# Kernel tuning notes

Measured on AMD Instinct MI355X. Metric: run time of the kernel, lower is better.

Reference implementation:

```python
import jax, jax.numpy as jnp
import numpy as np
import math

R1 = 1.0
R2 = 4.0
NBINS_XY = 4
NBINS_ZY = 4
PARTITIONS = NBINS_XY * NBINS_ZY * 2  # 32
TOPK = 200
TWO_PI = 2.0 * math.pi
PI = math.pi


def setup_inputs() -> dict:
    key = jax.random.key(0)
    k1, k2 = jax.random.split(key)
    # LiDAR-like coordinates, ~[-30, 30] meters
    sampled_vehicle_points = jax.random.normal(k1, (1024, 3), dtype=jnp.float32) * 20.0
    fusion_point = jax.random.normal(k2, (20000, 3), dtype=jnp.float32) * 20.0
    return {"sampled_vehicle_points": sampled_vehicle_points, "fusion_point": fusion_point}


def _compute_partitions_batch(q):
    # q: [S, K, 3]. rel[b, i, j] = q[b, j] - q[b, i]  (A.unsqueeze(1) - B.unsqueeze(2))
    rel = q[:, None, :, :] - q[:, :, None, :]  # [S, K, K, 3]
    angles_xy = jnp.fmod(jnp.arctan2(rel[..., 1], rel[..., 0]) + TWO_PI, TWO_PI)
    angles_zy = jnp.fmod(jnp.arctan2(rel[..., 1], rel[..., 2]) + TWO_PI, PI)
    xy_bins = jnp.floor(angles_xy / (TWO_PI / NBINS_XY))
    zy_bins = jnp.floor(angles_zy / (PI / NBINS_ZY))
    # hash(A, B, seed=NBINS_ZY): -1 where either < 0
    angle_ok = (xy_bins >= 0) & (zy_bins >= 0)
    angles_bins = jnp.where(angle_ok, xy_bins * NBINS_ZY + zy_bins, -1.0)
    D = jnp.sqrt(jnp.sum(rel * rel, axis=-1) + 1e-7)  # [S, K, K]
    dist_bins = jnp.where(D >= R2, 1.0, jnp.where(D >= R1, 0.0, -1.0))
    bin_ok = (dist_bins >= 0) & (angles_bins >= 0)
    bins = jnp.where(bin_ok, dist_bins * (NBINS_XY * NBINS_ZY) + angles_bins, -1.0)
    return bins  # [S, K, K] float, -1 for ignored


def reference(sampled_vehicle_points, fusion_point):
    # kNN query: K nearest fusion points for each sampled vehicle point
    d2 = jnp.sum(
        (sampled_vehicle_points[:, None, :] - fusion_point[None, :, :]) ** 2, axis=-1
    )  # [S, Nf]
    _, idx = jax.lax.top_k(-d2, TOPK)  # indices of TOPK smallest distances
    queried = fusion_point[idx]  # [S, K, 3]

    bins = _compute_partitions_batch(queried)  # [S, K, K]
    row0 = bins[:, 0, :]  # [S, K] — only row 0 is used by the loss
    # points_in_partition[s, p] = sum_j (row0[s, j] == p) + 1
    counts = jnp.sum(
        row0[:, :, None] == jnp.arange(PARTITIONS, dtype=bins.dtype)[None, None, :],
        axis=1,
    ).astype(jnp.float32) + 1.0  # [S, P]
    pip = counts / jnp.linalg.norm(counts, axis=-1, keepdims=True) * 4.0
    gt_dist = jax.nn.softmax(pip, axis=-1)
    return gt_dist
```

## Files before the change

kernel.cpp:

```cpp
#include <hip/hip_runtime.h>
#include <math.h>

#define KTOP 200
#define NPART 32
#define BLOCK 512
#define NHIST 2048
#define CAND_CAP 512
#define WCAP 512
#define MAXIT 10

__device__ __forceinline__ float d2_ref(float ax, float ay, float az,
                                        float bx, float by, float bz) {
    float dx = __fsub_rn(ax, bx), dy = __fsub_rn(ay, by), dz = __fsub_rn(az, bz);
    return __fadd_rn(__fadd_rn(__fmul_rn(dx, dx), __fmul_rn(dy, dy)), __fmul_rn(dz, dz));
}

__device__ __forceinline__ unsigned key_of(const float* __restrict__ fus, int j,
                                           float vx, float vy, float vz) {
    return __float_as_uint(d2_ref(vx, vy, vz, fus[3*j], fus[3*j+1], fus[3*j+2]));
}

__device__ __forceinline__ int compute_bin(float rx, float ry, float rz) {
    const float TWO_PI_F = (float)6.283185307179586;
    const float PI_F     = (float)3.141592653589793;
    const float XY_W     = (float)(6.283185307179586 / 4.0);
    const float ZY_W     = (float)(3.141592653589793 / 4.0);

    float d2 = __fadd_rn(__fadd_rn(__fmul_rn(rx, rx), __fmul_rn(ry, ry)), __fmul_rn(rz, rz));
    float D  = sqrtf(__fadd_rn(d2, 1e-7f));
    float dist_bin;
    if (D >= 4.0f)      dist_bin = 1.0f;
    else if (D >= 1.0f) dist_bin = 0.0f;
    else                return -1;

    float axy = fmodf(atan2f(ry, rx) + TWO_PI_F, TWO_PI_F);
    float azy = fmodf(atan2f(ry, rz) + TWO_PI_F, PI_F);
    float xyb = floorf(__fdiv_rn(axy, XY_W));
    float zyb = floorf(__fdiv_rn(azy, ZY_W));
    if (!(xyb >= 0.0f && zyb >= 0.0f)) return -1;
    float ab  = xyb * 4.0f + zyb;
    int bin = (int)(dist_bin * 16.0f + ab);
    return bin;
}

__global__ __launch_bounds__(BLOCK, 8)
void shape_context_kernel(const float* __restrict__ veh,
                          const float* __restrict__ fus,
                          float* __restrict__ out,
                          int nfus) {
    const int b   = blockIdx.x;
    const int tid = threadIdx.x;
    const int lane = tid & 63;
    const int wid  = tid >> 6;

    __shared__ unsigned int hist[NHIST];
    __shared__ unsigned long long cand[CAND_CAP];
    __shared__ int wlist[WCAP];
    __shared__ unsigned int hist32[NPART];
    __shared__ unsigned int waveTot[BLOCK / 64];
    __shared__ unsigned int waveBase[BLOCK / 64];
    __shared__ unsigned int s_bucket, s_rem, s_bcount;
    __shared__ int s_candCount, s_wcount;
    __shared__ float s_q0[3];
    __shared__ unsigned long long s_minPacked, s_lowBound;

    const float vx = veh[b * 3 + 0], vy = veh[b * 3 + 1], vz = veh[b * 3 + 2];
    const float4* fus4 = (const float4*)fus;
    const int ntrip = nfus >> 2;

    if (tid == 0) { s_minPacked = ~0ull; s_candCount = 0; s_wcount = 0; }
    for (int i = tid; i < NHIST; i += BLOCK) hist[i] = 0;
    if (tid < NPART) hist32[tid] = 0;
    __syncthreads();

    auto find_bucket = [&](unsigned remq) {
        const int PER = NHIST / BLOCK;
        int base = tid * PER;
        unsigned p = 0;
        #pragma unroll
        for (int i = 0; i < PER; i++) p += hist[base + i];
        unsigned incl = p;
        #pragma unroll
        for (int d = 1; d < 64; d <<= 1) {
            unsigned n = __shfl_up(incl, d, 64);
            if (lane >= d) incl += n;
        }
        if (lane == 63) waveTot[wid] = incl;
        __syncthreads();
        if (tid == 0) {
            unsigned acc = 0;
            for (int w = 0; w < BLOCK / 64; w++) { waveBase[w] = acc; acc += waveTot[w]; }
        }
        __syncthreads();
        unsigned excl = waveBase[wid] + incl - p;
        if (excl < remq && remq <= excl + p) {
            unsigned cum = excl;
            #pragma unroll
            for (int i = 0; i < PER; i++) {
                unsigned c = hist[base + i];
                if (cum + c >= remq) { s_bucket = base + i; s_rem = remq - cum; s_bcount = c; break; }
                cum += c;
            }
        }
        __syncthreads();
    };

    unsigned long long khi[MAXIT];
    unsigned long long lmin = ~0ull;
    #pragma unroll
    for (int it = 0; it < MAXIT; ++it) {
        int m = tid + it * BLOCK;
        if (m < ntrip) {
            float4 A = fus4[3 * m], Bq = fus4[3 * m + 1], Cq = fus4[3 * m + 2];
            unsigned k0 = __float_as_uint(d2_ref(vx, vy, vz, A.x,  A.y,  A.z));
            unsigned k1 = __float_as_uint(d2_ref(vx, vy, vz, A.w,  Bq.x, Bq.y));
            unsigned k2 = __float_as_uint(d2_ref(vx, vy, vz, Bq.z, Bq.w, Cq.x));
            unsigned k3 = __float_as_uint(d2_ref(vx, vy, vz, Cq.y, Cq.z, Cq.w));
            atomicAdd(&hist[k0 >> 21], 1u);
            atomicAdd(&hist[k1 >> 21], 1u);
            atomicAdd(&hist[k2 >> 21], 1u);
            atomicAdd(&hist[k3 >> 21], 1u);
            khi[it] = (unsigned long long)(k0 >> 21)
                    | ((unsigned long long)(k1 >> 21) << 16)
                    | ((unsigned long long)(k2 >> 21) << 32)
                    | ((unsigned long long)(k3 >> 21) << 48);
            unsigned jb = 4 * m;
            unsigned long long p0 = ((unsigned long long)k0 << 32) | (jb + 0);
            unsigned long long p1 = ((unsigned long long)k1 << 32) | (jb + 1);
            unsigned long long p2 = ((unsigned long long)k2 << 32) | (jb + 2);
            unsigned long long p3 = ((unsigned long long)k3 << 32) | (jb + 3);
            unsigned long long pm = min(min(p0, p1), min(p2, p3));
            lmin = min(lmin, pm);
        } else {
            khi[it] = 0xFFFFFFFFFFFFFFFFull;
        }
    }
    for (int m = MAXIT * BLOCK + tid; m < ntrip; m += BLOCK) {
        #pragma unroll
        for (int q = 0; q < 4; ++q) {
            unsigned k = key_of(fus, 4 * m + q, vx, vy, vz);
            atomicAdd(&hist[k >> 21], 1u);
            lmin = min(lmin, ((unsigned long long)k << 32) | (unsigned)(4 * m + q));
        }
    }
    for (int j = (nfus & ~3) + tid; j < nfus; j += BLOCK) {
        unsigned k = key_of(fus, j, vx, vy, vz);
        atomicAdd(&hist[k >> 21], 1u);
        lmin = min(lmin, ((unsigned long long)k << 32) | (unsigned)j);
    }
    #pragma unroll
    for (int d = 32; d > 0; d >>= 1) {
        unsigned long long o = __shfl_xor(lmin, d, 64);
        lmin = (o < lmin) ? o : lmin;
    }
    if (lane == 0) atomicMin(&s_minPacked, lmin);
    __syncthreads();

    find_bucket(KTOP);
    unsigned T = s_bucket;
    unsigned rem = s_rem;
    unsigned bcount = s_bcount;
    int shift = 21;

    if (tid == 0) {
        int idx0 = (int)(s_minPacked & 0xFFFFFFFFull);
        s_q0[0] = fus[idx0 * 3]; s_q0[1] = fus[idx0 * 3 + 1]; s_q0[2] = fus[idx0 * 3 + 2];
    }
    __syncthreads();
    const float q0x = s_q0[0], q0y = s_q0[1], q0z = s_q0[2];

    while (bcount > CAND_CAP && shift > 0) {
        int newshift = (shift > 11) ? (shift - 11) : 0;
        unsigned digmask = (1u << (shift - newshift)) - 1;
        for (int i = tid; i < NHIST; i += BLOCK) hist[i] = 0;
        __syncthreads();
        for (int j = tid; j < nfus; j += BLOCK) {
            unsigned k = key_of(fus, j, vx, vy, vz);
            if ((k >> shift) == T) atomicAdd(&hist[(k >> newshift) & digmask], 1u);
        }
        __syncthreads();
        find_bucket(rem);
        T = (T << (shift - newshift)) | s_bucket;
        rem = s_rem;
        bcount = s_bcount;
        shift = newshift;
    }

    if (shift == 21) {
        #pragma unroll
        for (int it = 0; it < MAXIT; ++it) {
            unsigned long long packed = khi[it];
            int jb = 4 * (tid + it * BLOCK);
            #pragma unroll
            for (int q = 0; q < 4; ++q) {
                unsigned hi = (unsigned)((packed >> (16 * q)) & 0xFFFFull);
                if (hi < T) {
                    int pos = atomicAdd(&s_wcount, 1);
                    if (pos < WCAP) wlist[pos] = jb + q;
                } else if (hi == T) {
                    int j = jb + q;
                    unsigned k = key_of(fus, j, vx, vy, vz);
                    int pos = atomicAdd(&s_candCount, 1);
                    if (pos < CAND_CAP) cand[pos] = ((unsigned long long)k << 32) | (unsigned)j;
                }
            }
        }
        for (int m = MAXIT * BLOCK + tid; m < ntrip; m += BLOCK)
            #pragma unroll
            for (int q = 0; q < 4; ++q) {
                int j = 4 * m + q;
                unsigned k = key_of(fus, j, vx, vy, vz);
                unsigned hi = k >> shift;
                if (hi < T) { int pos = atomicAdd(&s_wcount, 1); if (pos < WCAP) wlist[pos] = j; }
                else if (hi == T) { int pos = atomicAdd(&s_candCount, 1); if (pos < CAND_CAP) cand[pos] = ((unsigned long long)k << 32) | (unsigned)j; }
            }
        for (int j = (nfus & ~3) + tid; j < nfus; j += BLOCK) {
            unsigned k = key_of(fus, j, vx, vy, vz);
            unsigned hi = k >> shift;
            if (hi < T) { int pos = atomicAdd(&s_wcount, 1); if (pos < WCAP) wlist[pos] = j; }
            else if (hi == T) { int pos = atomicAdd(&s_candCount, 1); if (pos < CAND_CAP) cand[pos] = ((unsigned long long)k << 32) | (unsigned)j; }
        }
    } else {
        for (int j = tid; j < nfus; j += BLOCK) {
            unsigned k = key_of(fus, j, vx, vy, vz);
            unsigned hi = k >> shift;
            if (hi < T) { int pos = atomicAdd(&s_wcount, 1); if (pos < WCAP) wlist[pos] = j; }
            else if (hi == T) { int pos = atomicAdd(&s_candCount, 1); if (pos < CAND_CAP) cand[pos] = ((unsigned long long)k << 32) | (unsigned)j; }
        }
    }
    __syncthreads();

    const int cnt = s_candCount;
    if (cnt <= CAND_CAP) {
        for (int i = tid; i < cnt; i += BLOCK) {
            unsigned long long me = cand[i];
            int rank = 0;
            for (int k2 = 0; k2 < cnt; k2++) rank += (cand[k2] < me) ? 1 : 0;
            if (rank < (int)rem) {
                int pos = atomicAdd(&s_wcount, 1);
                if (pos < WCAP) wlist[pos] = (int)(me & 0xFFFFFFFFull);
            }
        }
    }
    __syncthreads();

    {
        int wc = s_wcount; if (wc > WCAP) wc = WCAP;
        for (int i = tid; i < wc; i += BLOCK) {
            int j = wlist[i];
            float fx = fus[3 * j], fy = fus[3 * j + 1], fz = fus[3 * j + 2];
            int bin = compute_bin(__fsub_rn(fx, q0x), __fsub_rn(fy, q0y), __fsub_rn(fz, q0z));
            if (bin >= 0 && bin < NPART) atomicAdd(&hist32[bin], 1u);
        }
    }
    __syncthreads();

    if (cnt > CAND_CAP) {
        if (tid == 0) s_lowBound = 0;
        __syncthreads();
        for (unsigned itx = 0; itx < rem; ++itx) {
            if (tid == 0) s_minPacked = ~0ull;
            __syncthreads();
            unsigned long long lowB = s_lowBound;
            unsigned long long lm = ~0ull;
            for (int j = tid; j < nfus; j += BLOCK) {
                unsigned k = key_of(fus, j, vx, vy, vz);
                if ((k >> shift) == T) {
                    unsigned long long p = ((unsigned long long)k << 32) | (unsigned)j;
                    if (p >= lowB && p < lm) lm = p;
                }
            }
            #pragma unroll
            for (int d = 32; d > 0; d >>= 1) {
                unsigned long long o = __shfl_xor(lm, d, 64);
                lm = (o < lm) ? o : lm;
            }
            if (lane == 0) atomicMin(&s_minPacked, lm);
            __syncthreads();
            if (tid == 0) {
                int jm = (int)(s_minPacked & 0xFFFFFFFFull);
                float fx = fus[jm * 3], fy = fus[jm * 3 + 1], fz = fus[jm * 3 + 2];
                int bin = compute_bin(__fsub_rn(fx, q0x), __fsub_rn(fy, q0y), __fsub_rn(fz, q0z));
                if (bin >= 0 && bin < NPART) hist32[bin] += 1u;
                s_lowBound = s_minPacked + 1;
            }
            __syncthreads();
        }
    }

    if (tid < NPART) {
        float c = (float)hist32[tid] + 1.0f;
        float ss = __fmul_rn(c, c);
        #pragma unroll
        for (int d = 16; d > 0; d >>= 1) ss += __shfl_xor(ss, d, 64);
        float v = __fmul_rn(__fdiv_rn(c, sqrtf(ss)), 4.0f);
        float mx = v;
        #pragma unroll
        for (int d = 16; d > 0; d >>= 1) mx = fmaxf(mx, __shfl_xor(mx, d, 64));
        float e = expf(v - mx);
        float sum = e;
        #pragma unroll
        for (int d = 16; d > 0; d >>= 1) sum += __shfl_xor(sum, d, 64);
        out[b * NPART + tid] = __fdiv_rn(e, sum);
    }
}

extern "C" void kernel_launch(void* const* d_in, const int* in_sizes, int n_in,
                              void* d_out, int out_size, void* d_ws, size_t ws_size,
                              hipStream_t stream) {
    const float* veh = (const float*)d_in[0];
    const float* fus = (const float*)d_in[1];
    float* out = (float*)d_out;
    int nveh = in_sizes[0] / 3;
    int nfus = in_sizes[1] / 3;
    shape_context_kernel<<<nveh, BLOCK, 0, stream>>>(veh, fus, out, nfus);
}
```

Measured before the change: 82.68 us.

## Split histogram per half-wave and derive nearest point from first bucket

Duplicates the shared-memory radix histogram into two copies selected by the upper half of each wave, which spreads out atomic contention. The per-element 64-bit running minimum in the main pass is dropped. The nearest point is instead found after the histogram pass by rescanning only elements in the first non-empty bucket with shared atomicMin. The candidate cap is also raised to 1024 so the refinement passes trigger less often, at the cost of more shared memory and a larger rank sort.

```diff
diff --git a/kernel.cpp b/kernel.cpp
--- a/kernel.cpp
+++ b/kernel.cpp
@@ -5,7 +5,8 @@
 #define NPART 32
 #define BLOCK 512
 #define NHIST 2048
-#define CAND_CAP 512
+#define HOFF 2049
+#define CAND_CAP 1024
 #define WCAP 512
 #define MAXIT 10
 
@@ -53,32 +54,33 @@
     const int lane = tid & 63;
     const int wid  = tid >> 6;
 
-    __shared__ unsigned int hist[NHIST];
+    __shared__ unsigned int hist[2 * NHIST + 1];
     __shared__ unsigned long long cand[CAND_CAP];
     __shared__ int wlist[WCAP];
     __shared__ unsigned int hist32[NPART];
     __shared__ unsigned int waveTot[BLOCK / 64];
     __shared__ unsigned int waveBase[BLOCK / 64];
-    __shared__ unsigned int s_bucket, s_rem, s_bcount;
+    __shared__ unsigned int s_bucket, s_rem, s_bcount, s_b0;
     __shared__ int s_candCount, s_wcount;
-    __shared__ float s_q0[3];
     __shared__ unsigned long long s_minPacked, s_lowBound;
 
     const float vx = veh[b * 3 + 0], vy = veh[b * 3 + 1], vz = veh[b * 3 + 2];
     const float4* fus4 = (const float4*)fus;
     const int ntrip = nfus >> 2;
+    const int hoff = (lane & 32) ? HOFF : 0;
 
     if (tid == 0) { s_minPacked = ~0ull; s_candCount = 0; s_wcount = 0; }
-    for (int i = tid; i < NHIST; i += BLOCK) hist[i] = 0;
+    for (int i = tid; i < 2 * NHIST + 1; i += BLOCK) hist[i] = 0;
     if (tid < NPART) hist32[tid] = 0;
     __syncthreads();
 
     auto find_bucket = [&](unsigned remq) {
         const int PER = NHIST / BLOCK;
         int base = tid * PER;
+        unsigned c[PER];
         unsigned p = 0;
         #pragma unroll
-        for (int i = 0; i < PER; i++) p += hist[base + i];
+        for (int i = 0; i < PER; i++) { c[i] = hist[base + i] + hist[HOFF + base + i]; p += c[i]; }
         unsigned incl = p;
         #pragma unroll
         for (int d = 1; d < 64; d <<= 1) {
@@ -93,20 +95,22 @@
         }
         __syncthreads();
         unsigned excl = waveBase[wid] + incl - p;
+        if (excl == 0 && p > 0) {
+            #pragma unroll
+            for (int i = 0; i < PER; i++) if (c[i] > 0) { s_b0 = base + i; break; }
+        }
         if (excl < remq && remq <= excl + p) {
             unsigned cum = excl;
             #pragma unroll
             for (int i = 0; i < PER; i++) {
-                unsigned c = hist[base + i];
-                if (cum + c >= remq) { s_bucket = base + i; s_rem = remq - cum; s_bcount = c; break; }
-                cum += c;
+                if (cum + c[i] >= remq) { s_bucket = base + i; s_rem = remq - cum; s_bcount = c[i]; break; }
+                cum += c[i];
             }
         }
         __syncthreads();
     };
 
     unsigned long long khi[MAXIT];
-    unsigned long long lmin = ~0ull;
     #pragma unroll
     for (int it = 0; it < MAXIT; ++it) {
         int m = tid + it * BLOCK;
@@ -116,67 +120,67 @@
             unsigned k1 = __float_as_uint(d2_ref(vx, vy, vz, A.w,  Bq.x, Bq.y));
             unsigned k2 = __float_as_uint(d2_ref(vx, vy, vz, Bq.z, Bq.w, Cq.x));
             unsigned k3 = __float_as_uint(d2_ref(vx, vy, vz, Cq.y, Cq.z, Cq.w));
-            atomicAdd(&hist[k0 >> 21], 1u);
-            atomicAdd(&hist[k1 >> 21], 1u);
-            atomicAdd(&hist[k2 >> 21], 1u);
-            atomicAdd(&hist[k3 >> 21], 1u);
+            atomicAdd(&hist[hoff + (k0 >> 21)], 1u);
+            atomicAdd(&hist[hoff + (k1 >> 21)], 1u);
+            atomicAdd(&hist[hoff + (k2 >> 21)], 1u);
+            atomicAdd(&hist[hoff + (k3 >> 21)], 1u);
             khi[it] = (unsigned long long)(k0 >> 21)
                     | ((unsigned long long)(k1 >> 21) << 16)
                     | ((unsigned long long)(k2 >> 21) << 32)
                     | ((unsigned long long)(k3 >> 21) << 48);
-            unsigned jb = 4 * m;
-            unsigned long long p0 = ((unsigned long long)k0 << 32) | (jb + 0);
-            unsigned long long p1 = ((unsigned long long)k1 << 32) | (jb + 1);
-            unsigned long long p2 = ((unsigned long long)k2 << 32) | (jb + 2);
-            unsigned long long p3 = ((unsigned long long)k3 << 32) | (jb + 3);
-            unsigned long long pm = min(min(p0, p1), min(p2, p3));
-            lmin = min(lmin, pm);
         } else {
             khi[it] = 0xFFFFFFFFFFFFFFFFull;
         }
     }
-    for (int m = MAXIT * BLOCK + tid; m < ntrip; m += BLOCK) {
-        #pragma unroll
-        for (int q = 0; q < 4; ++q) {
-            unsigned k = key_of(fus, 4 * m + q, vx, vy, vz);
-            atomicAdd(&hist[k >> 21], 1u);
-            lmin = min(lmin, ((unsigned long long)k << 32) | (unsigned)(4 * m + q));
-        }
-    }
-    for (int j = (nfus & ~3) + tid; j < nfus; j += BLOCK) {
-        unsigned k = key_of(fus, j, vx, vy, vz);
-        atomicAdd(&hist[k >> 21], 1u);
-        lmin = min(lmin, ((unsigned long long)k << 32) | (unsigned)j);
-    }
-    #pragma unroll
-    for (int d = 32; d > 0; d >>= 1) {
-        unsigned long long o = __shfl_xor(lmin, d, 64);
-        lmin = (o < lmin) ? o : lmin;
-    }
-    if (lane == 0) atomicMin(&s_minPacked, lmin);
+    for (int m = MAXIT * BLOCK + tid; m < ntrip; m += BLOCK)
+        #pragma unroll
+        for (int q = 0; q < 4; ++q)
+            atomicAdd(&hist[hoff + (key_of(fus, 4 * m + q, vx, vy, vz) >> 21)], 1u);
+    for (int j = (nfus & ~3) + tid; j < nfus; j += BLOCK)
+        atomicAdd(&hist[hoff + (key_of(fus, j, vx, vy, vz) >> 21)], 1u);
     __syncthreads();
 
     find_bucket(KTOP);
     unsigned T = s_bucket;
     unsigned rem = s_rem;
     unsigned bcount = s_bcount;
+    const unsigned b0 = s_b0;
     int shift = 21;
 
-    if (tid == 0) {
-        int idx0 = (int)(s_minPacked & 0xFFFFFFFFull);
-        s_q0[0] = fus[idx0 * 3]; s_q0[1] = fus[idx0 * 3 + 1]; s_q0[2] = fus[idx0 * 3 + 2];
-    }
-    __syncthreads();
-    const float q0x = s_q0[0], q0y = s_q0[1], q0z = s_q0[2];
+    #pragma unroll
+    for (int it = 0; it < MAXIT; ++it) {
+        unsigned long long packed = khi[it];
+        int jb = 4 * (tid + it * BLOCK);
+        #pragma unroll
+        for (int q = 0; q < 4; ++q) {
+            unsigned hi = (unsigned)((packed >> (16 * q)) & 0xFFFFull);
+            if (hi == b0) {
+                int j = jb + q;
+                unsigned k = key_of(fus, j, vx, vy, vz);
+                atomicMin(&s_minPacked, ((unsigned long long)k << 32) | (unsigned)j);
+            }
+        }
+    }
+    for (int m = MAXIT * BLOCK + tid; m < ntrip; m += BLOCK)
+        #pragma unroll
+        for (int q = 0; q < 4; ++q) {
+            unsigned k = key_of(fus, 4 * m + q, vx, vy, vz);
+            if ((k >> 21) == b0) atomicMin(&s_minPacked, ((unsigned long long)k << 32) | (unsigned)(4 * m + q));
+        }
+    for (int j = (nfus & ~3) + tid; j < nfus; j += BLOCK) {
+        unsigned k = key_of(fus, j, vx, vy, vz);
+        if ((k >> 21) == b0) atomicMin(&s_minPacked, ((unsigned long long)k << 32) | (unsigned)j);
+    }
 
     while (bcount > CAND_CAP && shift > 0) {
         int newshift = (shift > 11) ? (shift - 11) : 0;
         unsigned digmask = (1u << (shift - newshift)) - 1;
-        for (int i = tid; i < NHIST; i += BLOCK) hist[i] = 0;
+        __syncthreads();
+        for (int i = tid; i < 2 * NHIST + 1; i += BLOCK) hist[i] = 0;
         __syncthreads();
         for (int j = tid; j < nfus; j += BLOCK) {
             unsigned k = key_of(fus, j, vx, vy, vz);
-            if ((k >> shift) == T) atomicAdd(&hist[(k >> newshift) & digmask], 1u);
+            if ((k >> shift) == T) atomicAdd(&hist[hoff + ((k >> newshift) & digmask)], 1u);
         }
         __syncthreads();
         find_bucket(rem);
@@ -244,6 +248,9 @@
     }
     __syncthreads();
 
+    const int idx0 = (int)(s_minPacked & 0xFFFFFFFFull);
+    const float q0x = fus[idx0 * 3], q0y = fus[idx0 * 3 + 1], q0z = fus[idx0 * 3 + 2];
+
     {
         int wc = s_wcount; if (wc > WCAP) wc = WCAP;
         for (int i = tid; i < wc; i += BLOCK) {
@@ -253,7 +260,6 @@
             if (bin >= 0 && bin < NPART) atomicAdd(&hist32[bin], 1u);
         }
     }
-    __syncthreads();
 
     if (cnt > CAND_CAP) {
         if (tid == 0) s_lowBound = 0;
@@ -287,6 +293,7 @@
             __syncthreads();
         }
     }
+    __syncthreads();
 
     if (tid < NPART) {
         float c = (float)hist32[tid] + 1.0f;
```

Result: slower. 88.51 us (+7.1%).

## Sample-based threshold prefilter for top-k selection replacing full histogram pass

Applied to the files above, without the earlier changes.

Builds a coarse histogram from 512 evenly spaced sample points and picks a threshold bucket expected to hold a little more than the 200 nearest points. One pass over all fusion points then keeps only candidates under that threshold, and selection (min, histogram on finer bits, rank) runs on that small set in shared memory. This removes the full-data histogram with its global atomics and the per-thread packed key registers. A fallback path repeats the old full radix-select if the candidate count falls outside [KTOP, CAND_CAP], at extra cost for unlucky inputs.

```diff
diff --git a/kernel.cpp b/kernel.cpp
--- a/kernel.cpp
+++ b/kernel.cpp
@@ -5,9 +5,10 @@
 #define NPART 32
 #define BLOCK 512
 #define NHIST 2048
-#define CAND_CAP 512
-#define WCAP 512
-#define MAXIT 10
+#define CAND_CAP 2048
+#define TLIST_CAP 1024
+#define WCAP 256
+#define SSTAR 28
 
 __device__ __forceinline__ float d2_ref(float ax, float ay, float az,
                                         float bx, float by, float bz) {
@@ -55,20 +56,20 @@
 
     __shared__ unsigned int hist[NHIST];
     __shared__ unsigned long long cand[CAND_CAP];
+    __shared__ unsigned long long tlist[TLIST_CAP];
     __shared__ int wlist[WCAP];
     __shared__ unsigned int hist32[NPART];
     __shared__ unsigned int waveTot[BLOCK / 64];
     __shared__ unsigned int waveBase[BLOCK / 64];
     __shared__ unsigned int s_bucket, s_rem, s_bcount;
-    __shared__ int s_candCount, s_wcount;
-    __shared__ float s_q0[3];
-    __shared__ unsigned long long s_minPacked, s_lowBound;
+    __shared__ int s_candCount, s_wcount, s_tcount;
+    __shared__ unsigned long long s_minPacked, s_serMin, s_lowBound;
 
     const float vx = veh[b * 3 + 0], vy = veh[b * 3 + 1], vz = veh[b * 3 + 2];
     const float4* fus4 = (const float4*)fus;
     const int ntrip = nfus >> 2;
 
-    if (tid == 0) { s_minPacked = ~0ull; s_candCount = 0; s_wcount = 0; }
+    if (tid == 0) { s_minPacked = ~0ull; s_candCount = 0; s_wcount = 0; s_tcount = 0; }
     for (int i = tid; i < NHIST; i += BLOCK) hist[i] = 0;
     if (tid < NPART) hist32[tid] = 0;
     __syncthreads();
@@ -76,9 +77,10 @@
     auto find_bucket = [&](unsigned remq) {
         const int PER = NHIST / BLOCK;
         int base = tid * PER;
+        unsigned c[PER];
         unsigned p = 0;
         #pragma unroll
-        for (int i = 0; i < PER; i++) p += hist[base + i];
+        for (int i = 0; i < PER; i++) { c[i] = hist[base + i]; p += c[i]; }
         unsigned incl = p;
         #pragma unroll
         for (int d = 1; d < 64; d <<= 1) {
@@ -97,153 +99,205 @@
             unsigned cum = excl;
             #pragma unroll
             for (int i = 0; i < PER; i++) {
-                unsigned c = hist[base + i];
-                if (cum + c >= remq) { s_bucket = base + i; s_rem = remq - cum; s_bcount = c; break; }
-                cum += c;
+                if (cum + c[i] >= remq) { s_bucket = base + i; s_rem = remq - cum; s_bcount = c[i]; break; }
+                cum += c[i];
             }
         }
         __syncthreads();
     };
 
-    unsigned long long khi[MAXIT];
-    unsigned long long lmin = ~0ull;
-    #pragma unroll
-    for (int it = 0; it < MAXIT; ++it) {
-        int m = tid + it * BLOCK;
-        if (m < ntrip) {
-            float4 A = fus4[3 * m], Bq = fus4[3 * m + 1], Cq = fus4[3 * m + 2];
-            unsigned k0 = __float_as_uint(d2_ref(vx, vy, vz, A.x,  A.y,  A.z));
-            unsigned k1 = __float_as_uint(d2_ref(vx, vy, vz, A.w,  Bq.x, Bq.y));
-            unsigned k2 = __float_as_uint(d2_ref(vx, vy, vz, Bq.z, Bq.w, Cq.x));
-            unsigned k3 = __float_as_uint(d2_ref(vx, vy, vz, Cq.y, Cq.z, Cq.w));
-            atomicAdd(&hist[k0 >> 21], 1u);
-            atomicAdd(&hist[k1 >> 21], 1u);
-            atomicAdd(&hist[k2 >> 21], 1u);
-            atomicAdd(&hist[k3 >> 21], 1u);
-            khi[it] = (unsigned long long)(k0 >> 21)
-                    | ((unsigned long long)(k1 >> 21) << 16)
-                    | ((unsigned long long)(k2 >> 21) << 32)
-                    | ((unsigned long long)(k3 >> 21) << 48);
-            unsigned jb = 4 * m;
-            unsigned long long p0 = ((unsigned long long)k0 << 32) | (jb + 0);
-            unsigned long long p1 = ((unsigned long long)k1 << 32) | (jb + 1);
-            unsigned long long p2 = ((unsigned long long)k2 << 32) | (jb + 2);
-            unsigned long long p3 = ((unsigned long long)k3 << 32) | (jb + 3);
-            unsigned long long pm = min(min(p0, p1), min(p2, p3));
-            lmin = min(lmin, pm);
-        } else {
-            khi[it] = 0xFFFFFFFFFFFFFFFFull;
-        }
-    }
-    for (int m = MAXIT * BLOCK + tid; m < ntrip; m += BLOCK) {
-        #pragma unroll
-        for (int q = 0; q < 4; ++q) {
-            unsigned k = key_of(fus, 4 * m + q, vx, vy, vz);
-            atomicAdd(&hist[k >> 21], 1u);
-            lmin = min(lmin, ((unsigned long long)k << 32) | (unsigned)(4 * m + q));
-        }
+    {
+        int j = (int)(((long long)tid * nfus) / BLOCK);
+        unsigned k = key_of(fus, j, vx, vy, vz);
+        atomicAdd(&hist[k >> 21], 1u);
+    }
+    __syncthreads();
+    find_bucket(SSTAR);
+    const unsigned Pb = s_bucket + 1;
+    __syncthreads();
+
+    for (int m = tid; m < ntrip; m += BLOCK) {
+        float4 A = fus4[3 * m], Bq = fus4[3 * m + 1], Cq = fus4[3 * m + 2];
+        unsigned k0 = __float_as_uint(d2_ref(vx, vy, vz, A.x,  A.y,  A.z));
+        unsigned k1 = __float_as_uint(d2_ref(vx, vy, vz, A.w,  Bq.x, Bq.y));
+        unsigned k2 = __float_as_uint(d2_ref(vx, vy, vz, Bq.z, Bq.w, Cq.x));
+        unsigned k3 = __float_as_uint(d2_ref(vx, vy, vz, Cq.y, Cq.z, Cq.w));
+        int jb = 4 * m;
+        if ((k0 >> 21) < Pb) { int pos = atomicAdd(&s_candCount, 1); if (pos < CAND_CAP) cand[pos] = ((unsigned long long)k0 << 32) | (unsigned)(jb + 0); }
+        if ((k1 >> 21) < Pb) { int pos = atomicAdd(&s_candCount, 1); if (pos < CAND_CAP) cand[pos] = ((unsigned long long)k1 << 32) | (unsigned)(jb + 1); }
+        if ((k2 >> 21) < Pb) { int pos = atomicAdd(&s_candCount, 1); if (pos < CAND_CAP) cand[pos] = ((unsigned long long)k2 << 32) | (unsigned)(jb + 2); }
+        if ((k3 >> 21) < Pb) { int pos = atomicAdd(&s_candCount, 1); if (pos < CAND_CAP) cand[pos] = ((unsigned long long)k3 << 32) | (unsigned)(jb + 3); }
     }
     for (int j = (nfus & ~3) + tid; j < nfus; j += BLOCK) {
         unsigned k = key_of(fus, j, vx, vy, vz);
-        atomicAdd(&hist[k >> 21], 1u);
-        lmin = min(lmin, ((unsigned long long)k << 32) | (unsigned)j);
-    }
-    #pragma unroll
-    for (int d = 32; d > 0; d >>= 1) {
-        unsigned long long o = __shfl_xor(lmin, d, 64);
-        lmin = (o < lmin) ? o : lmin;
-    }
-    if (lane == 0) atomicMin(&s_minPacked, lmin);
-    __syncthreads();
-
-    find_bucket(KTOP);
-    unsigned T = s_bucket;
-    unsigned rem = s_rem;
-    unsigned bcount = s_bcount;
-    int shift = 21;
-
-    if (tid == 0) {
-        int idx0 = (int)(s_minPacked & 0xFFFFFFFFull);
-        s_q0[0] = fus[idx0 * 3]; s_q0[1] = fus[idx0 * 3 + 1]; s_q0[2] = fus[idx0 * 3 + 2];
-    }
-    __syncthreads();
-    const float q0x = s_q0[0], q0y = s_q0[1], q0z = s_q0[2];
-
-    while (bcount > CAND_CAP && shift > 0) {
-        int newshift = (shift > 11) ? (shift - 11) : 0;
-        unsigned digmask = (1u << (shift - newshift)) - 1;
+        if ((k >> 21) < Pb) { int pos = atomicAdd(&s_candCount, 1); if (pos < CAND_CAP) cand[pos] = ((unsigned long long)k << 32) | (unsigned)j; }
+    }
+    __syncthreads();
+
+    const int cnt = s_candCount;
+    unsigned rem;
+
+    if (cnt >= KTOP && cnt <= CAND_CAP) {
+        unsigned long long lm = ~0ull;
+        for (int i = tid; i < cnt; i += BLOCK) lm = min(lm, cand[i]);
+        #pragma unroll
+        for (int d = 32; d > 0; d >>= 1) {
+            unsigned long long o = __shfl_xor(lm, d, 64);
+            lm = (o < lm) ? o : lm;
+        }
+        if (lane == 0) atomicMin(&s_minPacked, lm);
+
         for (int i = tid; i < NHIST; i += BLOCK) hist[i] = 0;
         __syncthreads();
-        for (int j = tid; j < nfus; j += BLOCK) {
-            unsigned k = key_of(fus, j, vx, vy, vz);
-            if ((k >> shift) == T) atomicAdd(&hist[(k >> newshift) & digmask], 1u);
-        }
-        __syncthreads();
-        find_bucket(rem);
-        T = (T << (shift - newshift)) | s_bucket;
+        for (int i = tid; i < cnt; i += BLOCK) atomicAdd(&hist[(unsigned)(cand[i] >> 53)], 1u);
+        __syncthreads();
+        find_bucket(KTOP);
+        const unsigned T2 = s_bucket;
         rem = s_rem;
-        bcount = s_bcount;
-        shift = newshift;
-    }
-
-    if (shift == 21) {
-        #pragma unroll
-        for (int it = 0; it < MAXIT; ++it) {
-            unsigned long long packed = khi[it];
-            int jb = 4 * (tid + it * BLOCK);
-            #pragma unroll
-            for (int q = 0; q < 4; ++q) {
-                unsigned hi = (unsigned)((packed >> (16 * q)) & 0xFFFFull);
-                if (hi < T) {
+        const unsigned bcount = s_bcount;
+
+        if (bcount <= TLIST_CAP) {
+            for (int i = tid; i < cnt; i += BLOCK) {
+                unsigned bk = (unsigned)(cand[i] >> 53);
+                if (bk < T2) {
                     int pos = atomicAdd(&s_wcount, 1);
-                    if (pos < WCAP) wlist[pos] = jb + q;
-                } else if (hi == T) {
-                    int j = jb + q;
-                    unsigned k = key_of(fus, j, vx, vy, vz);
-                    int pos = atomicAdd(&s_candCount, 1);
-                    if (pos < CAND_CAP) cand[pos] = ((unsigned long long)k << 32) | (unsigned)j;
-                }
-            }
-        }
-        for (int m = MAXIT * BLOCK + tid; m < ntrip; m += BLOCK)
-            #pragma unroll
-            for (int q = 0; q < 4; ++q) {
-                int j = 4 * m + q;
+                    if (pos < WCAP) wlist[pos] = (int)(cand[i] & 0xFFFFFFFFull);
+                } else if (bk == T2) {
+                    int pos = atomicAdd(&s_tcount, 1);
+                    if (pos < TLIST_CAP) tlist[pos] = cand[i];
+                }
+            }
+            __syncthreads();
+            const int tc = s_tcount;
+            for (int i = tid; i < tc; i += BLOCK) {
+                unsigned long long me = tlist[i];
+                int rank = 0;
+                for (int k2 = 0; k2 < tc; k2++) rank += (tlist[k2] < me) ? 1 : 0;
+                if (rank < (int)rem) {
+                    int pos = atomicAdd(&s_wcount, 1);
+                    if (pos < WCAP) wlist[pos] = (int)(me & 0xFFFFFFFFull);
+                }
+            }
+        } else {
+            for (int i = tid; i < cnt; i += BLOCK) {
+                unsigned bk = (unsigned)(cand[i] >> 53);
+                if (bk < T2) {
+                    int pos = atomicAdd(&s_wcount, 1);
+                    if (pos < WCAP) wlist[pos] = (int)(cand[i] & 0xFFFFFFFFull);
+                }
+            }
+            __syncthreads();
+            for (int i = tid; i < cnt; i += BLOCK) {
+                unsigned long long me = cand[i];
+                if ((unsigned)(me >> 53) == T2) {
+                    int rank = 0;
+                    for (int k2 = 0; k2 < cnt; k2++) {
+                        unsigned long long o = cand[k2];
+                        rank += ((unsigned)(o >> 53) == T2 && o < me) ? 1 : 0;
+                    }
+                    if (rank < (int)rem) {
+                        int pos = atomicAdd(&s_wcount, 1);
+                        if (pos < WCAP) wlist[pos] = (int)(me & 0xFFFFFFFFull);
+                    }
+                }
+            }
+        }
+        __syncthreads();
+    } else {
+        if (tid == 0) s_candCount = 0;
+        for (int i = tid; i < NHIST; i += BLOCK) hist[i] = 0;
+        __syncthreads();
+        for (int j = tid; j < nfus; j += BLOCK)
+            atomicAdd(&hist[key_of(fus, j, vx, vy, vz) >> 21], 1u);
+        __syncthreads();
+        find_bucket(KTOP);
+        unsigned T = s_bucket;
+        rem = s_rem;
+        unsigned bcount = s_bcount;
+        int shift = 21;
+
+        while (bcount > CAND_CAP && shift > 0) {
+            int newshift = (shift > 11) ? (shift - 11) : 0;
+            unsigned digmask = (1u << (shift - newshift)) - 1;
+            __syncthreads();
+            for (int i = tid; i < NHIST; i += BLOCK) hist[i] = 0;
+            __syncthreads();
+            for (int j = tid; j < nfus; j += BLOCK) {
                 unsigned k = key_of(fus, j, vx, vy, vz);
-                unsigned hi = k >> shift;
-                if (hi < T) { int pos = atomicAdd(&s_wcount, 1); if (pos < WCAP) wlist[pos] = j; }
-                else if (hi == T) { int pos = atomicAdd(&s_candCount, 1); if (pos < CAND_CAP) cand[pos] = ((unsigned long long)k << 32) | (unsigned)j; }
-            }
-        for (int j = (nfus & ~3) + tid; j < nfus; j += BLOCK) {
-            unsigned k = key_of(fus, j, vx, vy, vz);
-            unsigned hi = k >> shift;
-            if (hi < T) { int pos = atomicAdd(&s_wcount, 1); if (pos < WCAP) wlist[pos] = j; }
-            else if (hi == T) { int pos = atomicAdd(&s_candCount, 1); if (pos < CAND_CAP) cand[pos] = ((unsigned long long)k << 32) | (unsigned)j; }
-        }
-    } else {
+                if ((k >> shift) == T) atomicAdd(&hist[(k >> newshift) & digmask], 1u);
+            }
+            __syncthreads();
+            find_bucket(rem);
+            T = (T << (shift - newshift)) | s_bucket;
+            rem = s_rem;
+            bcount = s_bcount;
+            shift = newshift;
+        }
+
         for (int j = tid; j < nfus; j += BLOCK) {
             unsigned k = key_of(fus, j, vx, vy, vz);
             unsigned hi = k >> shift;
-            if (hi < T) { int pos = atomicAdd(&s_wcount, 1); if (pos < WCAP) wlist[pos] = j; }
-            else if (hi == T) { int pos = atomicAdd(&s_candCount, 1); if (pos < CAND_CAP) cand[pos] = ((unsigned long long)k << 32) | (unsigned)j; }
-        }
-    }
-    __syncthreads();
-
-    const int cnt = s_candCount;
-    if (cnt <= CAND_CAP) {
-        for (int i = tid; i < cnt; i += BLOCK) {
-            unsigned long long me = cand[i];
-            int rank = 0;
-            for (int k2 = 0; k2 < cnt; k2++) rank += (cand[k2] < me) ? 1 : 0;
-            if (rank < (int)rem) {
+            if (hi < T) {
                 int pos = atomicAdd(&s_wcount, 1);
-                if (pos < WCAP) wlist[pos] = (int)(me & 0xFFFFFFFFull);
-            }
-        }
-    }
-    __syncthreads();
-
+                if (pos < WCAP) wlist[pos] = j;
+                atomicMin(&s_minPacked, ((unsigned long long)k << 32) | (unsigned)j);
+            } else if (hi == T) {
+                int pos = atomicAdd(&s_candCount, 1);
+                if (pos < CAND_CAP) cand[pos] = ((unsigned long long)k << 32) | (unsigned)j;
+                atomicMin(&s_minPacked, ((unsigned long long)k << 32) | (unsigned)j);
+            }
+        }
+        __syncthreads();
+        const int fcnt = s_candCount;
+        if (fcnt <= CAND_CAP) {
+            for (int i = tid; i < fcnt; i += BLOCK) {
+                unsigned long long me = cand[i];
+                int rank = 0;
+                for (int k2 = 0; k2 < fcnt; k2++) rank += (cand[k2] < me) ? 1 : 0;
+                if (rank < (int)rem) {
+                    int pos = atomicAdd(&s_wcount, 1);
+                    if (pos < WCAP) wlist[pos] = (int)(me & 0xFFFFFFFFull);
+                }
+            }
+            __syncthreads();
+        } else {
+            const int idx0f = (int)(s_minPacked & 0xFFFFFFFFull);
+            const float fq0x = fus[idx0f * 3], fq0y = fus[idx0f * 3 + 1], fq0z = fus[idx0f * 3 + 2];
+            if (tid == 0) s_lowBound = 0;
+            __syncthreads();
+            for (unsigned itx = 0; itx < rem; ++itx) {
+                if (tid == 0) s_serMin = ~0ull;
+                __syncthreads();
+                unsigned long long lowB = s_lowBound;
+                unsigned long long lmx = ~0ull;
+                for (int j = tid; j < nfus; j += BLOCK) {
+                    unsigned k = key_of(fus, j, vx, vy, vz);
+                    if ((k >> shift) == T) {
+                        unsigned long long p = ((unsigned long long)k << 32) | (unsigned)j;
+                        if (p >= lowB && p < lmx) lmx = p;
+                    }
+                }
+                #pragma unroll
+                for (int d = 32; d > 0; d >>= 1) {
+                    unsigned long long o = __shfl_xor(lmx, d, 64);
+                    lmx = (o < lmx) ? o : lmx;
+                }
+                if (lane == 0) atomicMin(&s_serMin, lmx);
+                __syncthreads();
+                if (tid == 0) {
+                    int jm = (int)(s_serMin & 0xFFFFFFFFull);
+                    float fx = fus[jm * 3], fy = fus[jm * 3 + 1], fz = fus[jm * 3 + 2];
+                    int bin = compute_bin(__fsub_rn(fx, fq0x), __fsub_rn(fy, fq0y), __fsub_rn(fz, fq0z));
+                    if (bin >= 0 && bin < NPART) hist32[bin] += 1u;
+                    s_lowBound = s_serMin + 1;
+                }
+                __syncthreads();
+            }
+        }
+    }
+
+    const int idx0 = (int)(s_minPacked & 0xFFFFFFFFull);
+    const float q0x = fus[idx0 * 3], q0y = fus[idx0 * 3 + 1], q0z = fus[idx0 * 3 + 2];
     {
         int wc = s_wcount; if (wc > WCAP) wc = WCAP;
         for (int i = tid; i < wc; i += BLOCK) {
@@ -254,39 +308,6 @@
         }
     }
     __syncthreads();
-
-    if (cnt > CAND_CAP) {
-        if (tid == 0) s_lowBound = 0;
-        __syncthreads();
-        for (unsigned itx = 0; itx < rem; ++itx) {
-            if (tid == 0) s_minPacked = ~0ull;
-            __syncthreads();
-            unsigned long long lowB = s_lowBound;
-            unsigned long long lm = ~0ull;
-            for (int j = tid; j < nfus; j += BLOCK) {
-                unsigned k = key_of(fus, j, vx, vy, vz);
-                if ((k >> shift) == T) {
-                    unsigned long long p = ((unsigned long long)k << 32) | (unsigned)j;
-                    if (p >= lowB && p < lm) lm = p;
-                }
-            }
-            #pragma unroll
-            for (int d = 32; d > 0; d >>= 1) {
-                unsigned long long o = __shfl_xor(lm, d, 64);
-                lm = (o < lm) ? o : lm;
-            }
-            if (lane == 0) atomicMin(&s_minPacked, lm);
-            __syncthreads();
-            if (tid == 0) {
-                int jm = (int)(s_minPacked & 0xFFFFFFFFull);
-                float fx = fus[jm * 3], fy = fus[jm * 3 + 1], fz = fus[jm * 3 + 2];
-                int bin = compute_bin(__fsub_rn(fx, q0x), __fsub_rn(fy, q0y), __fsub_rn(fz, q0z));
-                if (bin >= 0 && bin < NPART) hist32[bin] += 1u;
-                s_lowBound = s_minPacked + 1;
-            }
-            __syncthreads();
-        }
-    }
 
     if (tid < NPART) {
         float c = (float)hist32[tid] + 1.0f;
```

Measured after the change: 89.98 us. 8.8% more time.
